# Performance work log

Measured on AMD Instinct MI355X. Metric: run time of the kernel, lower is better.

The kernel has to match this reference:

```python
import jax, jax.numpy as jnp
import numpy as np
from jax import lax

B, T, I = 256, 720, 16   # batch, seq_len, input_dim
H = 128                  # hidden_dim
PRED_LEN = 96


def lstm_cell(x, h, c, W_ih, W_hh, b):
    # PyTorch gate order: i, f, g, o ; b = b_ih + b_hh (combined)
    gates = x @ W_ih.T + h @ W_hh.T + b
    i, f, g, o = jnp.split(gates, 4, axis=-1)
    c = jax.nn.sigmoid(f) * c + jax.nn.sigmoid(i) * jnp.tanh(g)
    h = jax.nn.sigmoid(o) * jnp.tanh(c)
    return h, c


def setup_inputs() -> dict:
    key = jax.random.key(0)
    ks = jax.random.split(key, 16)
    k = 1.0 / np.sqrt(H)
    u = lambda kk, shape: jax.random.uniform(kk, shape, jnp.float32, -k, k)
    inp = {
        "x": jax.random.normal(ks[0], (B, T, I), jnp.float32),
        # encoder (bidirectional, 1 layer): forward + backward directions
        "e_Wih_f": u(ks[1], (4 * H, I)), "e_Whh_f": u(ks[2], (4 * H, H)), "e_b_f": u(ks[3], (4 * H,)),
        "e_Wih_b": u(ks[4], (4 * H, I)), "e_Whh_b": u(ks[5], (4 * H, H)), "e_b_b": u(ks[6], (4 * H,)),
        # decoder (bidirectional, 1 layer)
        "d_Wih_f": u(ks[7], (4 * H, I)), "d_Whh_f": u(ks[8], (4 * H, H)), "d_b_f": u(ks[9], (4 * H,)),
        "d_Wih_b": u(ks[10], (4 * H, I)), "d_Whh_b": u(ks[11], (4 * H, H)), "d_b_b": u(ks[12], (4 * H,)),
        # final linear: (2H -> I)
        "W_lin": u(ks[13], (I, 2 * H)), "b_lin": u(ks[14], (I,)),
    }
    return inp


def reference(x, e_Wih_f, e_Whh_f, e_b_f, e_Wih_b, e_Whh_b, e_b_b,
              d_Wih_f, d_Whh_f, d_b_f, d_Wih_b, d_Whh_b, d_b_b,
              W_lin, b_lin):
    xt = jnp.transpose(x, (1, 0, 2))  # [T, B, I] time-major
    h0 = jnp.zeros((B, H), x.dtype)
    c0 = jnp.zeros((B, H), x.dtype)

    # ---- encoder: bidirectional LSTM; only final (h, c) per direction is used ----
    def enc_f(carry, xt_t):
        h, c = lstm_cell(xt_t, carry[0], carry[1], e_Wih_f, e_Whh_f, e_b_f)
        return (h, c), None

    def enc_b(carry, xt_t):
        h, c = lstm_cell(xt_t, carry[0], carry[1], e_Wih_b, e_Whh_b, e_b_b)
        return (h, c), None

    (hf, cf), _ = lax.scan(enc_f, (h0, c0), xt)
    (hb, cb), _ = lax.scan(enc_b, (h0, c0), xt[::-1])

    def dec_step(carry, _):
        inp, hf, cf, hb, cb = carry
        hf, cf = lstm_cell(inp, hf, cf, d_Wih_f, d_Whh_f, d_b_f)
        hb, cb = lstm_cell(inp, hb, cb, d_Wih_b, d_Whh_b, d_b_b)
        # seq_len==1 so out_f = forward hidden, out_b = backward hidden
        out = jnp.concatenate([hf, hb], axis=-1) @ W_lin.T + b_lin  # [B, I]
        return (out, hf, cf, hb, cb), out

    init = (x[:, -1, :], hf, cf, hb, cb)
    _, outs = lax.scan(dec_step, init, None, length=PRED_LEN)  # [P, B, I]
    return jnp.transpose(outs, (1, 0, 2))  # [B, pred_len, I]
```

## Files before the change

kernel.cpp:

```cpp
#include <hip/hip_runtime.h>
#include <math.h>

#define TB    720
#define NI    16
#define NH    128
#define NG    512
#define PRED  96
#define CHUNK 90

typedef _Float16 h2    __attribute__((ext_vector_type(2)));
typedef _Float16 f16x4 __attribute__((ext_vector_type(4)));
typedef _Float16 f16x8 __attribute__((ext_vector_type(8)));
typedef float    f32x4 __attribute__((ext_vector_type(4)));

#define LOG2E  1.4426950408889634f
#define LOG2E2 2.8853900817779268f

__device__ __forceinline__ float rcpf_(float v) {
#if __has_builtin(__builtin_amdgcn_rcpf)
    return __builtin_amdgcn_rcpf(v);
#else
    return 1.0f / v;
#endif
}
__device__ __forceinline__ float ex2(float v) {
#if __has_builtin(__builtin_amdgcn_exp2f)
    return __builtin_amdgcn_exp2f(v);
#else
    return exp2f(v);
#endif
}
__device__ __forceinline__ float sigf(float v)   { return rcpf_(1.0f + __expf(-v)); }
__device__ __forceinline__ float tanhf_(float v) { return 1.0f - 2.0f * rcpf_(1.0f + __expf(2.0f * v)); }

__device__ __forceinline__ unsigned int packf16(float a, float b) {
    h2 p; p.x = (_Float16)a; p.y = (_Float16)b;
    return __builtin_bit_cast(unsigned int, p);
}
__device__ __forceinline__ float2 unpackf16(unsigned int u) {
    h2 p = __builtin_bit_cast(h2, u);
    return make_float2((float)p.x, (float)p.y);
}
__device__ __forceinline__ float fdot2f(unsigned int a, unsigned int b, float c) {
#if __has_builtin(__builtin_amdgcn_fdot2)
    return __builtin_amdgcn_fdot2(__builtin_bit_cast(h2, a), __builtin_bit_cast(h2, b), c, false);
#else
    h2 x = __builtin_bit_cast(h2, a), y = __builtin_bit_cast(h2, b);
    return c + (float)x.x * (float)y.x + (float)x.y * (float)y.y;
#endif
}

__device__ __forceinline__ f16x8 mk8s(const float* p, float s) {
    f16x8 v;
    v[0] = (_Float16)(p[0]  * s); v[1] = (_Float16)(p[1]  * s);
    v[2] = (_Float16)(p[2]  * s); v[3] = (_Float16)(p[3]  * s);
    v[4] = (_Float16)(p[16] * s); v[5] = (_Float16)(p[17] * s);
    v[6] = (_Float16)(p[18] * s); v[7] = (_Float16)(p[19] * s);
    return v;
}
__device__ __forceinline__ f32x4 MFMA(f16x8 a, f16x8 b, f32x4 c) {
    return __builtin_amdgcn_mfma_f32_16x16x32_f16(a, b, c, 0, 0, 0);
}

__global__ __launch_bounds__(512, 1)
void enc_kernel(const float* __restrict__ x,
                const float* __restrict__ Wih_f, const float* __restrict__ Whh_f, const float* __restrict__ b_f,
                const float* __restrict__ Wih_b, const float* __restrict__ Whh_b, const float* __restrict__ b_b,
                float* __restrict__ st)
{
    __shared__ _Float16 hbuf0[16 * NH];
    __shared__ _Float16 hbuf1[16 * NH];
    __shared__ unsigned int xsh[CHUNK * 128];

    const int blk = blockIdx.x;
    const int dir = blk & 1;
    const int b0  = (blk >> 1) << 4;
    const int t   = threadIdx.x;
    const int wv  = t >> 6;
    const int l   = t & 63;
    const int lr  = l & 15;
    const int lk  = l >> 4;

    const float* Wih = dir ? Wih_b : Wih_f;
    const float* Whh = dir ? Whh_b : Whh_f;
    const float* bv  = dir ? b_b   : b_f;

    const int mt0 = wv * 4, mt1 = wv * 4 + 1, mt2 = wv * 4 + 2, mt3 = wv * 4 + 3;
    const int R0 = mt0 * 16 + lr, R1 = mt1 * 16 + lr, R2 = mt2 * 16 + lr, R3 = mt3 * 16 + lr;
    const int or0 = (R0 & 3) * 128 + (R0 >> 2);
    const int or1 = (R1 & 3) * 128 + (R1 >> 2);
    const int or2 = (R2 & 3) * 128 + (R2 >> 2);
    const int or3 = (R3 & 3) * 128 + (R3 >> 2);
    const float s0 = ((or0 >> 7) == 2) ? LOG2E2 : LOG2E;
    const float s1 = ((or1 >> 7) == 2) ? LOG2E2 : LOG2E;
    const float s2 = ((or2 >> 7) == 2) ? LOG2E2 : LOG2E;
    const float s3 = ((or3 >> 7) == 2) ? LOG2E2 : LOG2E;
    const float* p0 = Whh + (size_t)or0 * NH + lk * 4;
    const float* p1 = Whh + (size_t)or1 * NH + lk * 4;
    const float* p2 = Whh + (size_t)or2 * NH + lk * 4;
    const float* p3 = Whh + (size_t)or3 * NH + lk * 4;
    f16x8 w0_0 = mk8s(p0, s0), w0_1 = mk8s(p0 + 32, s0), w0_2 = mk8s(p0 + 64, s0), w0_3 = mk8s(p0 + 96, s0);
    f16x8 w1_0 = mk8s(p1, s1), w1_1 = mk8s(p1 + 32, s1), w1_2 = mk8s(p1 + 64, s1), w1_3 = mk8s(p1 + 96, s1);
    f16x8 w2_0 = mk8s(p2, s2), w2_1 = mk8s(p2 + 32, s2), w2_2 = mk8s(p2 + 64, s2), w2_3 = mk8s(p2 + 96, s2);
    f16x8 w3_0 = mk8s(p3, s3), w3_1 = mk8s(p3 + 32, s3), w3_2 = mk8s(p3 + 64, s3), w3_3 = mk8s(p3 + 96, s3);

    f16x8 ax0, ax1, ax2, ax3;
#define MKAXR(DST, OR, SC) { \
    const float* xr_ = Wih + (size_t)(OR) * NI + lk * 4; \
    DST[0] = (_Float16)(xr_[0] * (SC)); DST[1] = (_Float16)(xr_[1] * (SC)); \
    DST[2] = (_Float16)(xr_[2] * (SC)); DST[3] = (_Float16)(xr_[3] * (SC)); \
    DST[4] = (_Float16)(bv[(OR)] * (SC)); \
    DST[5] = (_Float16)0.f; DST[6] = (_Float16)0.f; DST[7] = (_Float16)0.f; }
    MKAXR(ax0, or0, s0) MKAXR(ax1, or1, s1) MKAXR(ax2, or2, s2) MKAXR(ax3, or3, s3)
#undef MKAXR

    const int d0 = mt0 * 4 + lk, d1 = mt1 * 4 + lk, d2 = mt2 * 4 + lk, d3 = mt3 * 4 + lk;

    ((unsigned int*)hbuf0)[t] = 0u;
    ((unsigned int*)hbuf0)[t + 512] = 0u;
    float cs0 = 0.f, cs1 = 0.f, cs2 = 0.f, cs3 = 0.f;

    const int hro0 = 0 * 1024 + lk * 256 + lr * 16;
    const int hro1 = 1 * 1024 + lk * 256 + lr * 16;
    const int hro2 = 2 * 1024 + lk * 256 + lr * 16;
    const int hro3 = 3 * 1024 + lk * 256 + lr * 16;
#define CWB(D) ((((D) >> 5) * 1024) + ((((D) & 15) >> 2) * 256) + lr * 16 + (((((D) & 31) >> 4) * 4 + ((D) & 3)) * 2))
    const int cwb0 = CWB(d0), cwb1 = CWB(d1), cwb2 = CWB(d2), cwb3 = CWB(d3);
#undef CWB
    const int xoff = lk * 128 + lr * 8;
    f16x8 bxT;
    bxT[0] = (_Float16)0.f; bxT[1] = (_Float16)0.f; bxT[2] = (_Float16)0.f; bxT[3] = (_Float16)0.f;
    bxT[4] = (lk == 0) ? (_Float16)1.0f : (_Float16)0.f;
    bxT[5] = (_Float16)0.f; bxT[6] = (_Float16)0.f; bxT[7] = (_Float16)0.f;
    const f32x4 CZ = {0.f, 0.f, 0.f, 0.f};
    __syncthreads();

#define CELL(J, HW) { \
    float ei_ = ex2(-C##J[0]), ef_ = ex2(-C##J[1]); \
    float eg_ = ex2(C##J[2]),  eo_ = ex2(-C##J[3]); \
    float di_ = 1.f + ei_, df_ = 1.f + ef_, dg_ = 1.f + eg_, dq_ = 1.f + eo_; \
    float r1_ = rcpf_(di_ * df_), r2_ = rcpf_(dq_ * dg_); \
    float si_ = r1_ * df_, sf_ = r1_ * di_, so_ = r2_ * dg_; \
    float tg_ = __builtin_fmaf(-2.f * r2_, dq_, 1.f); \
    cs##J = sf_ * cs##J + si_ * tg_; \
    float ec_ = ex2(cs##J * LOG2E2); \
    float th_ = __builtin_fmaf(-2.f, rcpf_(1.f + ec_), 1.f); \
    float hv_ = so_ * th_; \
    *(_Float16*)((char*)(HW) + cwb##J) = (_Float16)hv_; }

#define STEP(HR, HW, SI) { \
    const char* hrb_ = (const char*)(HR); \
    f16x8 bh0 = *(const f16x8*)(hrb_ + hro0); \
    f16x8 bh1 = *(const f16x8*)(hrb_ + hro1); \
    f16x8 bh2 = *(const f16x8*)(hrb_ + hro2); \
    f16x8 bh3 = *(const f16x8*)(hrb_ + hro3); \
    f16x8 bx = bxT; \
    *(f16x4*)&bx = *(const f16x4*)((const char*)xsh + (SI) * 512 + xoff); \
    f32x4 C0 = MFMA(ax0, bx, CZ); f32x4 C1 = MFMA(ax1, bx, CZ); \
    f32x4 C2 = MFMA(ax2, bx, CZ); f32x4 C3 = MFMA(ax3, bx, CZ); \
    C0 = MFMA(w0_0, bh0, C0); C1 = MFMA(w1_0, bh0, C1); \
    C2 = MFMA(w2_0, bh0, C2); C3 = MFMA(w3_0, bh0, C3); \
    C0 = MFMA(w0_1, bh1, C0); C1 = MFMA(w1_1, bh1, C1); \
    C2 = MFMA(w2_1, bh1, C2); C3 = MFMA(w3_1, bh1, C3); \
    C0 = MFMA(w0_2, bh2, C0); C1 = MFMA(w1_2, bh2, C1); \
    C2 = MFMA(w2_2, bh2, C2); C3 = MFMA(w3_2, bh2, C3); \
    C0 = MFMA(w0_3, bh3, C0); C1 = MFMA(w1_3, bh3, C1); \
    C2 = MFMA(w2_3, bh3, C2); C3 = MFMA(w3_3, bh3, C3); \
    CELL(0, HW) CELL(1, HW) CELL(2, HW) CELL(3, HW) \
    __syncthreads(); }

    for (int c = 0; c < 8; ++c) {
        {
            const int c0 = c * CHUNK;
            for (int i = t; i < 16 * CHUNK * 8; i += 512) {
                const int br  = i / (CHUNK * 8);
                const int rem = i - br * (CHUNK * 8);
                const int ti  = rem >> 3;
                const int dw  = rem & 7;
                const int s_  = c0 + ti;
                const int tt  = dir ? (TB - 1 - s_) : s_;
                float2 v = *(const float2*)(x + ((size_t)(b0 + br) * TB + tt) * NI + dw * 2);
                xsh[ti * 128 + (dw >> 1) * 32 + br * 2 + (dw & 1)] = packf16(v.x, v.y);
            }
        }
        __syncthreads();
        for (int si2 = 0; si2 < CHUNK / 2; ++si2) {
            STEP(hbuf0, hbuf1, si2 * 2)
            STEP(hbuf1, hbuf0, si2 * 2 + 1)
        }
    }
#undef STEP
#undef CELL

    {
        const size_t base = ((size_t)(b0 + lr) * 2 + dir) * 2 * NH;
#define FIN(J) { \
        float hv_ = (float)*(const _Float16*)((const char*)hbuf0 + cwb##J); \
        st[base + d##J] = hv_; st[base + NH + d##J] = cs##J; }
        FIN(0) FIN(1) FIN(2) FIN(3)
#undef FIN
    }
}

#define R8(F)  F(0)F(1)F(2)F(3)F(4)F(5)F(6)F(7)
#define R36_(F) F(8)F(9)F(10)F(11)F(12)F(13)F(14)F(15)F(16)F(17)F(18)F(19)F(20)F(21)F(22)F(23)F(24)F(25)F(26)F(27)F(28)F(29)F(30)F(31)F(32)F(33)F(34)F(35)
#define R36(F) R8(F) R36_(F)
#define R64(F) R36(F) F(36)F(37)F(38)F(39)F(40)F(41)F(42)F(43)F(44)F(45)F(46)F(47)F(48)F(49)F(50)F(51)F(52)F(53)F(54)F(55)F(56)F(57)F(58)F(59)F(60)F(61)F(62)F(63)

#define QD(Q,i0,i1,i2,i3) { a0 = fdot2f((Q).x, w##i0, a0); a1 = fdot2f((Q).y, w##i1, a1); \
                            a2 = fdot2f((Q).z, w##i2, a2); a3 = fdot2f((Q).w, w##i3, a3); }
#define QDU(Q,i0,i1,i2,i3) { a0 = fdot2f((Q).x, u##i0, a0); a1 = fdot2f((Q).y, u##i1, a1); \
                             a2 = fdot2f((Q).z, u##i2, a2); a3 = fdot2f((Q).w, u##i3, a3); }

__global__ __launch_bounds__(1024, 1)
void dec_kernel(const float* __restrict__ x,
                const float* __restrict__ Wih_f, const float* __restrict__ Whh_f, const float* __restrict__ b_f,
                const float* __restrict__ Wih_b, const float* __restrict__ Whh_b, const float* __restrict__ b_b,
                const float* __restrict__ Wlin, const float* __restrict__ blin,
                const float* __restrict__ st, float* __restrict__ out)
{
    __shared__ unsigned int hFh[NH / 2], hBh[NH / 2];
    __shared__ unsigned int inpH[NI / 2];
    __shared__ float g[1024];
    __shared__ float obuf[PRED * 16];

    const int b    = blockIdx.x;
    const int t    = threadIdx.x;
    const int cell = t >> 9;
    const int r    = t & 511;
    const int w    = t >> 6;
    const int ln   = t & 63;

    const float* Wih = cell ? Wih_b : Wih_f;
    const float* Whh = cell ? Whh_b : Whh_f;
    const float* bv  = cell ? b_b   : b_f;

#define DW(K) unsigned int w##K;
    R64(DW)
#undef DW
#define DU(K) unsigned int u##K;
    R8(DU)
#undef DU
    {
        const float* xr = Wih + r * NI;
        const float* hr = Whh + r * NH;
#define LU(K) u##K = packf16(xr[2*(K)], xr[2*(K)+1]);
        R8(LU)
#undef LU
#define LH(K) w##K = packf16(hr[2*(K)], hr[2*(K)+1]);
        R64(LH)
#undef LH
    }
    const float bias = bv[r];

    const float wl0 = Wlin[w * 256 + ln * 4 + 0];
    const float wl1 = Wlin[w * 256 + ln * 4 + 1];
    const float wl2 = Wlin[w * 256 + ln * 4 + 2];
    const float wl3 = Wlin[w * 256 + ln * 4 + 3];
    const float blw = blin[w];

    float cc = 0.0f;
    if (t < 64) {
        const float* sh = st + ((b * 2 + 0) * 2 + 0) * NH;
        hFh[t] = packf16(sh[2 * t], sh[2 * t + 1]);
    } else if (t < 128) {
        const float* sh = st + ((b * 2 + 1) * 2 + 0) * NH;
        hBh[t - 64] = packf16(sh[2 * (t - 64)], sh[2 * (t - 64) + 1]);
    }
    if (t < NH) cc = st[((b * 2 + 0) * 2 + 1) * NH + t];
    else if (t >= 512 && t < 512 + NH) cc = st[((b * 2 + 1) * 2 + 1) * NH + (t - 512)];
    if (t < 8) {
        float2 v = ((const float2*)(x + (size_t)b * TB * NI + (TB - 1) * NI))[t];
        inpH[t] = packf16(v.x, v.y);
    }
    __syncthreads();

    for (int s = 0; s < PRED; ++s) {
        float a0 = bias, a1 = 0.f, a2 = 0.f, a3 = 0.f;
        uint4 q;
        {
            const uint4* xv = (const uint4*)inpH;
            q = xv[0]; QDU(q, 0, 1, 2, 3)
            q = xv[1]; QDU(q, 4, 5, 6, 7)
        }
        const uint4* hv = cell ? (const uint4*)hBh : (const uint4*)hFh;
        q = hv[0];  QD(q, 0, 1, 2, 3)
        q = hv[1];  QD(q, 4, 5, 6, 7)
        q = hv[2];  QD(q, 8, 9, 10, 11)
        q = hv[3];  QD(q, 12, 13, 14, 15)
        q = hv[4];  QD(q, 16, 17, 18, 19)
        q = hv[5];  QD(q, 20, 21, 22, 23)
        q = hv[6];  QD(q, 24, 25, 26, 27)
        q = hv[7];  QD(q, 28, 29, 30, 31)
        q = hv[8];  QD(q, 32, 33, 34, 35)
        q = hv[9];  QD(q, 36, 37, 38, 39)
        q = hv[10]; QD(q, 40, 41, 42, 43)
        q = hv[11]; QD(q, 44, 45, 46, 47)
        q = hv[12]; QD(q, 48, 49, 50, 51)
        q = hv[13]; QD(q, 52, 53, 54, 55)
        q = hv[14]; QD(q, 56, 57, 58, 59)
        q = hv[15]; QD(q, 60, 61, 62, 63)
        g[t] = (a0 + a1) + (a2 + a3);
        __syncthreads();

        if ((t < NH) || (t >= 512 && t < 512 + NH)) {
            float gi = g[t], gf = g[t + NH], gg = g[t + 2 * NH], go = g[t + 3 * NH];
            cc = sigf(gf) * cc + sigf(gi) * tanhf_(gg);
            float h = sigf(go) * tanhf_(cc);
            if (t < NH) ((_Float16*)hFh)[t] = (_Float16)h;
            else        ((_Float16*)hBh)[t - 512] = (_Float16)h;
        }
        __syncthreads();

        {
            const unsigned int* hsrc = (ln < 32) ? (hFh + 2 * ln) : (hBh + 2 * (ln - 32));
            uint2 hw = *(const uint2*)hsrc;
            float2 va = unpackf16(hw.x), vb = unpackf16(hw.y);
            float p = va.x * wl0 + va.y * wl1 + vb.x * wl2 + vb.y * wl3;
            p += __shfl_xor(p, 1);  p += __shfl_xor(p, 2);  p += __shfl_xor(p, 4);
            p += __shfl_xor(p, 8);  p += __shfl_xor(p, 16); p += __shfl_xor(p, 32);
            if (ln == 0) {
                float o = p + blw;
                obuf[s * NI + w] = o;
                ((_Float16*)inpH)[w] = (_Float16)o;
            }
        }
        __syncthreads();
    }

    {
        float4* dst = (float4*)(out + (size_t)b * PRED * NI);
        const float4* src = (const float4*)obuf;
        for (int i = t; i < PRED * NI / 4; i += 1024) dst[i] = src[i];
    }
}

extern "C" void kernel_launch(void* const* d_in, const int* in_sizes, int n_in,
                              void* d_out, int out_size, void* d_ws, size_t ws_size,
                              hipStream_t stream)
{
    const float* x      = (const float*)d_in[0];
    const float* eWih_f = (const float*)d_in[1];
    const float* eWhh_f = (const float*)d_in[2];
    const float* eb_f   = (const float*)d_in[3];
    const float* eWih_b = (const float*)d_in[4];
    const float* eWhh_b = (const float*)d_in[5];
    const float* eb_b   = (const float*)d_in[6];
    const float* dWih_f = (const float*)d_in[7];
    const float* dWhh_f = (const float*)d_in[8];
    const float* db_f   = (const float*)d_in[9];
    const float* dWih_b = (const float*)d_in[10];
    const float* dWhh_b = (const float*)d_in[11];
    const float* db_b   = (const float*)d_in[12];
    const float* Wlin   = (const float*)d_in[13];
    const float* blin   = (const float*)d_in[14];

    float* st = (float*)d_ws;

    enc_kernel<<<32, 512, 0, stream>>>(x, eWih_f, eWhh_f, eb_f, eWih_b, eWhh_b, eb_b, st);
    dec_kernel<<<256, 1024, 0, stream>>>(x, dWih_f, dWhh_f, db_f, dWih_b, dWhh_b, db_b,
                                         Wlin, blin, st, (float*)d_out);
}
```

Baseline: 804.1 us.

## Double encoder waves per block, stage input weights in LDS, use DPP reductions

The encoder block grows from 512 to 1024 threads, so each wave owns two gate M-tiles instead of four. This halves the MFMA chain and cell math per wave on the serial 720-step recurrence. The input-projection A fragments move from registers into LDS and are reloaded each step, with an opaque offset to stop the compiler hoisting them. The h fragment loads are interleaved with the MFMAs. In the decoder, the wave-wide shuffle-xor reduction becomes a DPP row_shr/row_bcast scan that ends in lane 63. The trade-off is more waves per barrier and extra LDS traffic on every step.

Result: faster. 751.6 us (-6.5%).

```diff
diff --git a/kernel.cpp b/kernel.cpp
--- a/kernel.cpp
+++ b/kernel.cpp
@@ -61,8 +61,16 @@
 __device__ __forceinline__ f32x4 MFMA(f16x8 a, f16x8 b, f32x4 c) {
     return __builtin_amdgcn_mfma_f32_16x16x32_f16(a, b, c, 0, 0, 0);
 }
-
-__global__ __launch_bounds__(512, 1)
+__device__ __forceinline__ int opaque(int v) { asm volatile("" : "+v"(v)); return v; }
+
+template <int CTRL, int RMASK>
+__device__ __forceinline__ float dppadd(float v) {
+    int s = __builtin_bit_cast(int, v);
+    int d = __builtin_amdgcn_update_dpp(0, s, CTRL, RMASK, 0xf, true);
+    return v + __builtin_bit_cast(float, d);
+}
+
+__global__ __launch_bounds__(1024, 4)
 void enc_kernel(const float* __restrict__ x,
                 const float* __restrict__ Wih_f, const float* __restrict__ Whh_f, const float* __restrict__ b_f,
                 const float* __restrict__ Wih_b, const float* __restrict__ Whh_b, const float* __restrict__ b_b,
@@ -71,6 +79,7 @@
     __shared__ _Float16 hbuf0[16 * NH];
     __shared__ _Float16 hbuf1[16 * NH];
     __shared__ unsigned int xsh[CHUNK * 128];
+    __shared__ uint4 axl[32 * 64];
 
     const int blk = blockIdx.x;
     const int dir = blk & 1;
@@ -85,53 +94,48 @@
     const float* Whh = dir ? Whh_b : Whh_f;
     const float* bv  = dir ? b_b   : b_f;
 
-    const int mt0 = wv * 4, mt1 = wv * 4 + 1, mt2 = wv * 4 + 2, mt3 = wv * 4 + 3;
-    const int R0 = mt0 * 16 + lr, R1 = mt1 * 16 + lr, R2 = mt2 * 16 + lr, R3 = mt3 * 16 + lr;
+    for (int e = t; e < 2048; e += 1024) {
+        const int mt = e >> 6, ll = e & 63;
+        const int elr = ll & 15, elk = ll >> 4;
+        const int R   = mt * 16 + elr;
+        const int orr = (R & 3) * 128 + (R >> 2);
+        const float sc = ((orr >> 7) == 2) ? LOG2E2 : LOG2E;
+        const float* xr = Wih + (size_t)orr * NI + elk * 4;
+        uint4 q;
+        q.x = packf16(xr[0] * sc, xr[1] * sc);
+        q.y = packf16(xr[2] * sc, xr[3] * sc);
+        q.z = packf16(bv[orr] * sc, 0.f);
+        q.w = 0u;
+        axl[mt * 64 + ll] = q;
+    }
+
+    const int mt0 = 2 * wv, mt1 = 2 * wv + 1;
+    const int R0 = mt0 * 16 + lr, R1 = mt1 * 16 + lr;
     const int or0 = (R0 & 3) * 128 + (R0 >> 2);
     const int or1 = (R1 & 3) * 128 + (R1 >> 2);
-    const int or2 = (R2 & 3) * 128 + (R2 >> 2);
-    const int or3 = (R3 & 3) * 128 + (R3 >> 2);
     const float s0 = ((or0 >> 7) == 2) ? LOG2E2 : LOG2E;
     const float s1 = ((or1 >> 7) == 2) ? LOG2E2 : LOG2E;
-    const float s2 = ((or2 >> 7) == 2) ? LOG2E2 : LOG2E;
-    const float s3 = ((or3 >> 7) == 2) ? LOG2E2 : LOG2E;
     const float* p0 = Whh + (size_t)or0 * NH + lk * 4;
     const float* p1 = Whh + (size_t)or1 * NH + lk * 4;
-    const float* p2 = Whh + (size_t)or2 * NH + lk * 4;
-    const float* p3 = Whh + (size_t)or3 * NH + lk * 4;
     f16x8 w0_0 = mk8s(p0, s0), w0_1 = mk8s(p0 + 32, s0), w0_2 = mk8s(p0 + 64, s0), w0_3 = mk8s(p0 + 96, s0);
     f16x8 w1_0 = mk8s(p1, s1), w1_1 = mk8s(p1 + 32, s1), w1_2 = mk8s(p1 + 64, s1), w1_3 = mk8s(p1 + 96, s1);
-    f16x8 w2_0 = mk8s(p2, s2), w2_1 = mk8s(p2 + 32, s2), w2_2 = mk8s(p2 + 64, s2), w2_3 = mk8s(p2 + 96, s2);
-    f16x8 w3_0 = mk8s(p3, s3), w3_1 = mk8s(p3 + 32, s3), w3_2 = mk8s(p3 + 64, s3), w3_3 = mk8s(p3 + 96, s3);
-
-    f16x8 ax0, ax1, ax2, ax3;
-#define MKAXR(DST, OR, SC) { \
-    const float* xr_ = Wih + (size_t)(OR) * NI + lk * 4; \
-    DST[0] = (_Float16)(xr_[0] * (SC)); DST[1] = (_Float16)(xr_[1] * (SC)); \
-    DST[2] = (_Float16)(xr_[2] * (SC)); DST[3] = (_Float16)(xr_[3] * (SC)); \
-    DST[4] = (_Float16)(bv[(OR)] * (SC)); \
-    DST[5] = (_Float16)0.f; DST[6] = (_Float16)0.f; DST[7] = (_Float16)0.f; }
-    MKAXR(ax0, or0, s0) MKAXR(ax1, or1, s1) MKAXR(ax2, or2, s2) MKAXR(ax3, or3, s3)
-#undef MKAXR
-
-    const int d0 = mt0 * 4 + lk, d1 = mt1 * 4 + lk, d2 = mt2 * 4 + lk, d3 = mt3 * 4 + lk;
+
+    const int d0 = mt0 * 4 + lk, d1 = mt1 * 4 + lk;
 
     ((unsigned int*)hbuf0)[t] = 0u;
-    ((unsigned int*)hbuf0)[t + 512] = 0u;
-    float cs0 = 0.f, cs1 = 0.f, cs2 = 0.f, cs3 = 0.f;
+    float cs0 = 0.f, cs1 = 0.f;
 
     const int hro0 = 0 * 1024 + lk * 256 + lr * 16;
     const int hro1 = 1 * 1024 + lk * 256 + lr * 16;
     const int hro2 = 2 * 1024 + lk * 256 + lr * 16;
     const int hro3 = 3 * 1024 + lk * 256 + lr * 16;
 #define CWB(D) ((((D) >> 5) * 1024) + ((((D) & 15) >> 2) * 256) + lr * 16 + (((((D) & 31) >> 4) * 4 + ((D) & 3)) * 2))
-    const int cwb0 = CWB(d0), cwb1 = CWB(d1), cwb2 = CWB(d2), cwb3 = CWB(d3);
+    const int cwb0 = CWB(d0), cwb1 = CWB(d1);
 #undef CWB
     const int xoff = lk * 128 + lr * 8;
-    f16x8 bxT;
-    bxT[0] = (_Float16)0.f; bxT[1] = (_Float16)0.f; bxT[2] = (_Float16)0.f; bxT[3] = (_Float16)0.f;
-    bxT[4] = (lk == 0) ? (_Float16)1.0f : (_Float16)0.f;
-    bxT[5] = (_Float16)0.f; bxT[6] = (_Float16)0.f; bxT[7] = (_Float16)0.f;
+    const int axo0 = (mt0 * 64 + l) * 16;
+    const int axo1 = (mt1 * 64 + l) * 16;
+    const unsigned int oneku = (lk == 0) ? 0x00003c00u : 0u;
     const f32x4 CZ = {0.f, 0.f, 0.f, 0.f};
     __syncthreads();
 
@@ -150,29 +154,30 @@
 
 #define STEP(HR, HW, SI) { \
     const char* hrb_ = (const char*)(HR); \
-    f16x8 bh0 = *(const f16x8*)(hrb_ + hro0); \
-    f16x8 bh1 = *(const f16x8*)(hrb_ + hro1); \
-    f16x8 bh2 = *(const f16x8*)(hrb_ + hro2); \
-    f16x8 bh3 = *(const f16x8*)(hrb_ + hro3); \
-    f16x8 bx = bxT; \
-    *(f16x4*)&bx = *(const f16x4*)((const char*)xsh + (SI) * 512 + xoff); \
-    f32x4 C0 = MFMA(ax0, bx, CZ); f32x4 C1 = MFMA(ax1, bx, CZ); \
-    f32x4 C2 = MFMA(ax2, bx, CZ); f32x4 C3 = MFMA(ax3, bx, CZ); \
-    C0 = MFMA(w0_0, bh0, C0); C1 = MFMA(w1_0, bh0, C1); \
-    C2 = MFMA(w2_0, bh0, C2); C3 = MFMA(w3_0, bh0, C3); \
-    C0 = MFMA(w0_1, bh1, C0); C1 = MFMA(w1_1, bh1, C1); \
-    C2 = MFMA(w2_1, bh1, C2); C3 = MFMA(w3_1, bh1, C3); \
-    C0 = MFMA(w0_2, bh2, C0); C1 = MFMA(w1_2, bh2, C1); \
-    C2 = MFMA(w2_2, bh2, C2); C3 = MFMA(w3_2, bh2, C3); \
-    C0 = MFMA(w0_3, bh3, C0); C1 = MFMA(w1_3, bh3, C1); \
-    C2 = MFMA(w2_3, bh3, C2); C3 = MFMA(w3_3, bh3, C3); \
-    CELL(0, HW) CELL(1, HW) CELL(2, HW) CELL(3, HW) \
+    f16x8 bx; \
+    { uint2 xq_ = *(const uint2*)((const char*)xsh + (SI) * 512 + xoff); \
+      ((unsigned int*)&bx)[0] = xq_.x; ((unsigned int*)&bx)[1] = xq_.y; \
+      ((unsigned int*)&bx)[2] = oneku; ((unsigned int*)&bx)[3] = 0u; } \
+    f16x8 ax0_ = *(const f16x8*)((const char*)axl + opaque(axo0)); \
+    f16x8 ax1_ = *(const f16x8*)((const char*)axl + opaque(axo1)); \
+    f32x4 C0 = MFMA(ax0_, bx, CZ); \
+    f32x4 C1 = MFMA(ax1_, bx, CZ); \
+    f16x8 bh_; \
+    bh_ = *(const f16x8*)(hrb_ + hro0); \
+    C0 = MFMA(w0_0, bh_, C0); C1 = MFMA(w1_0, bh_, C1); \
+    bh_ = *(const f16x8*)(hrb_ + hro1); \
+    C0 = MFMA(w0_1, bh_, C0); C1 = MFMA(w1_1, bh_, C1); \
+    bh_ = *(const f16x8*)(hrb_ + hro2); \
+    C0 = MFMA(w0_2, bh_, C0); C1 = MFMA(w1_2, bh_, C1); \
+    bh_ = *(const f16x8*)(hrb_ + hro3); \
+    C0 = MFMA(w0_3, bh_, C0); C1 = MFMA(w1_3, bh_, C1); \
+    CELL(0, HW) CELL(1, HW) \
     __syncthreads(); }
 
     for (int c = 0; c < 8; ++c) {
         {
             const int c0 = c * CHUNK;
-            for (int i = t; i < 16 * CHUNK * 8; i += 512) {
+            for (int i = t; i < 16 * CHUNK * 8; i += 1024) {
                 const int br  = i / (CHUNK * 8);
                 const int rem = i - br * (CHUNK * 8);
                 const int ti  = rem >> 3;
@@ -197,7 +202,7 @@
 #define FIN(J) { \
         float hv_ = (float)*(const _Float16*)((const char*)hbuf0 + cwb##J); \
         st[base + d##J] = hv_; st[base + NH + d##J] = cs##J; }
-        FIN(0) FIN(1) FIN(2) FIN(3)
+        FIN(0) FIN(1)
 #undef FIN
     }
 }
@@ -317,9 +322,13 @@
             uint2 hw = *(const uint2*)hsrc;
             float2 va = unpackf16(hw.x), vb = unpackf16(hw.y);
             float p = va.x * wl0 + va.y * wl1 + vb.x * wl2 + vb.y * wl3;
-            p += __shfl_xor(p, 1);  p += __shfl_xor(p, 2);  p += __shfl_xor(p, 4);
-            p += __shfl_xor(p, 8);  p += __shfl_xor(p, 16); p += __shfl_xor(p, 32);
-            if (ln == 0) {
+            p = dppadd<0x111, 0xf>(p);
+            p = dppadd<0x112, 0xf>(p);
+            p = dppadd<0x114, 0xf>(p);
+            p = dppadd<0x118, 0xf>(p);
+            p = dppadd<0x142, 0xa>(p);
+            p = dppadd<0x143, 0xc>(p);
+            if (ln == 63) {
                 float o = p + blw;
                 obuf[s * NI + w] = o;
                 ((_Float16*)inpH)[w] = (_Float16)o;
@@ -357,7 +366,7 @@
 
     float* st = (float*)d_ws;
 
-    enc_kernel<<<32, 512, 0, stream>>>(x, eWih_f, eWhh_f, eb_f, eWih_b, eWhh_b, eb_b, st);
+    enc_kernel<<<32, 1024, 0, stream>>>(x, eWih_f, eWhh_f, eb_f, eWih_b, eWhh_b, eb_b, st);
     dec_kernel<<<256, 1024, 0, stream>>>(x, dWih_f, dWhh_f, db_f, dWih_b, dWhh_b, db_b,
                                          Wlin, blin, st, (float*)d_out);
 }
```
